# Kernel tuning notes

Measured on AMD Instinct MI355X. Metric: run time of the kernel, lower is better.

The kernel has to match this reference:

```python
import jax, jax.numpy as jnp
import numpy as np

N_NODES = 50000
N_EDGES = 600000
N_FEAT = 128
N_GRAPHS = 256
DIM = 95
N_OUT = 12
N_ITER = 10
BN_EPS = 1e-5


def setup_inputs() -> dict:
    key = jax.random.key(0)
    ks = jax.random.split(key, 16)
    inp = {}
    inp["x"] = jax.random.normal(ks[0], (N_NODES, N_FEAT), dtype=jnp.float32)
    inp["edge_index"] = jax.random.randint(ks[1], (2, N_EDGES), 0, N_NODES, dtype=jnp.int64)
    inp["batch"] = jnp.sort(jax.random.randint(ks[2], (N_NODES,), 0, N_GRAPHS, dtype=jnp.int64))
    def lin(k, fan_in, fan_out):
        bound = 1.0 / np.sqrt(fan_in)
        kw, kb = jax.random.split(k)
        W = jax.random.uniform(kw, (fan_in, fan_out), jnp.float32, -bound, bound)
        b = jax.random.uniform(kb, (fan_out,), jnp.float32, -bound, bound)
        return W, b
    inp["W1a"], inp["b1a"] = lin(ks[3], N_FEAT, N_FEAT)            # nn1 layer 1
    inp["W1b"], inp["b1b"] = lin(ks[4], N_FEAT, N_FEAT)            # nn1 layer 2
    inp["gamma"] = jnp.ones((N_FEAT,), jnp.float32)                 # bn1 weight
    inp["beta"] = jnp.zeros((N_FEAT,), jnp.float32)                 # bn1 bias
    inp["Wl1"], inp["bl1"] = lin(ks[5], 2 * N_FEAT, N_FEAT // 2)   # lin1
    inp["Wl2"], inp["bl2"] = lin(ks[6], 2 * N_FEAT, N_FEAT // 2)   # lin2
    inp["Wm1"], inp["bm1"] = lin(ks[7], N_FEAT, DIM)               # MLP layer 1
    inp["Wm2"], inp["bm2"] = lin(ks[8], DIM, N_OUT)                # MLP layer 2
    return inp


def reference(x, edge_index, batch, W1a, b1a, W1b, b1b, gamma, beta,
              Wl1, bl1, Wl2, bl2, Wm1, bm1, Wm2, bm2):
    src, dst = edge_index[0], edge_index[1]
    # GINConv (eps=0): h_i = nn1(x_i + sum_{j->i} x_j)
    agg = jax.ops.segment_sum(x[src], dst, num_segments=N_NODES)
    h0 = x + agg
    h0 = jax.nn.relu(h0 @ W1a + b1a) @ W1b + b1b
    x1 = jax.nn.relu(h0)
    # BatchNorm1d (training mode: batch statistics, biased variance)
    mean = jnp.mean(x1, axis=0)
    var = jnp.mean(jnp.square(x1 - mean), axis=0)
    x1 = gamma * (x1 - mean) * jax.lax.rsqrt(var + BN_EPS) + beta
    # global_mean_pool over graph ids
    sums = jax.ops.segment_sum(x1, batch, num_segments=N_GRAPHS)
    counts = jax.ops.segment_sum(jnp.ones((N_NODES,), x1.dtype), batch, num_segments=N_GRAPHS)
    xg = sums / jnp.maximum(counts, 1.0)[:, None]
    # recurrent gated loop
    h = xg
    for _ in range(N_ITER):
        cat = jnp.concatenate([xg, h], axis=1)          # [G, 2*F]
        p = cat @ Wl1 + bl1
        q = cat @ Wl2 + bl2
        h = jnp.concatenate([jnp.tanh(q), jax.nn.sigmoid(p)], axis=1)
    # output MLP
    return jax.nn.relu(h @ Wm1 + bm1) @ Wm2 + bm2
```

## Files before the change

kernel.cpp:

```cpp
#include <hip/hip_runtime.h>
#include <cstddef>

#define N_NODES  50000
#define N_EDGES  600000
#define N_FEAT   128
#define N_GRAPHS 256
#define DIMM     95
#define N_OUTD   12
#define N_ITERS  10

#define N_CHUNKS 196

#define WS_STATS 0
#define WS_XG    (WS_STATS + 256)
#define WS_CNT   (WS_XG + N_GRAPHS * N_FEAT)
#define WS_OFF   (WS_CNT + N_NODES)
#define WS_CUR   (WS_OFF + N_NODES + 4)
#define WS_CHS   (WS_CUR + N_NODES)
#define WS_SORT  (WS_CHS + 256)

#define SR 132

__global__ void k_zero(float* __restrict__ ws) {
    int i = blockIdx.x * 256 + threadIdx.x;
    int* cnt = (int*)ws + WS_CNT;
    if (i < N_NODES) cnt[i] = 0;
    if (i < 256) ws[WS_STATS + i] = 0.f;
    if (i < N_GRAPHS * N_FEAT) ws[WS_XG + i] = 0.f;
}

__global__ void k_hist(const int* __restrict__ ei, float* __restrict__ ws) {
    int e = blockIdx.x * 256 + threadIdx.x;
    int* cnt = (int*)ws + WS_CNT;
    if (e < N_EDGES) atomicAdd(&cnt[ei[N_EDGES + e]], 1);
}

__global__ void k_chunk(float* __restrict__ ws) {
    __shared__ int red[4];
    const int tid = threadIdx.x;
    int* cnt = (int*)ws + WS_CNT;
    int i = blockIdx.x * 256 + tid;
    int v = (i < N_NODES) ? cnt[i] : 0;
    #pragma unroll
    for (int d = 32; d; d >>= 1) v += __shfl_down(v, d);
    if ((tid & 63) == 0) red[tid >> 6] = v;
    __syncthreads();
    if (tid == 0) ((int*)ws + WS_CHS)[blockIdx.x] = red[0] + red[1] + red[2] + red[3];
}

__global__ void k_scan0(float* __restrict__ ws) {
    __shared__ int s[256];
    const int tid = threadIdx.x;
    int* chs = (int*)ws + WS_CHS;
    int v = (tid < N_CHUNKS) ? chs[tid] : 0;
    s[tid] = v;
    __syncthreads();
    #pragma unroll
    for (int d = 1; d < 256; d <<= 1) {
        int t = (tid >= d) ? s[tid - d] : 0;
        __syncthreads();
        s[tid] += t;
        __syncthreads();
    }
    if (tid < N_CHUNKS) chs[tid] = s[tid] - v;
    if (tid == 0) ((int*)ws + WS_OFF)[N_NODES] = N_EDGES;
}

__global__ void k_scan1(float* __restrict__ ws) {
    __shared__ int s[256];
    const int tid = threadIdx.x;
    int* cnt = (int*)ws + WS_CNT;
    int* off = (int*)ws + WS_OFF;
    int* cur = (int*)ws + WS_CUR;
    int i = blockIdx.x * 256 + tid;
    int v = (i < N_NODES) ? cnt[i] : 0;
    s[tid] = v;
    __syncthreads();
    #pragma unroll
    for (int d = 1; d < 256; d <<= 1) {
        int t = (tid >= d) ? s[tid - d] : 0;
        __syncthreads();
        s[tid] += t;
        __syncthreads();
    }
    int o = ((int*)ws + WS_CHS)[blockIdx.x] + s[tid] - v;
    if (i < N_NODES) { off[i] = o; cur[i] = o; }
}

__global__ void k_scatter(const int* __restrict__ ei, float* __restrict__ ws) {
    int e = blockIdx.x * 256 + threadIdx.x;
    if (e >= N_EDGES) return;
    int d = ei[N_EDGES + e];
    int s = ei[e];
    int* cur = (int*)ws + WS_CUR;
    int pos = atomicAdd(&cur[d], 1);
    ((int*)ws + WS_SORT)[pos] = s;
}

__global__ __launch_bounds__(256, 4) void k_fused(const float* __restrict__ x,
        const int* __restrict__ batch, float* __restrict__ ws,
        const float* __restrict__ W1a, const float* __restrict__ b1a,
        const float* __restrict__ W1b, const float* __restrict__ b1b) {
    __shared__ float As[64 * SR];
    __shared__ float red[256];
    __shared__ int batch_l[64];
    const int tid  = threadIdx.x;
    const int lane = tid & 63;
    const int wv   = tid >> 6;
    const int fg   = tid & 15;
    const int rg   = tid >> 4;
    const int row0 = blockIdx.x * 64;

    const int* off = (const int*)ws + WS_OFF;
    const int* ss  = (const int*)ws + WS_SORT;

    if (tid < 64) {
        int r = row0 + tid;
        batch_l[tid] = (r < N_NODES) ? batch[r] : (N_GRAPHS - 1);
    }

    for (int ii = 0; ii < 16; ++ii) {
        const int i = wv * 16 + ii;
        const int r = row0 + i;
        float2 acc = make_float2(0.f, 0.f);
        if (r < N_NODES) {
            acc = *(const float2*)(x + (size_t)r * N_FEAT + 2 * lane);
            const int lo = off[r], hi = off[r + 1];
            for (int c0 = lo; c0 < hi; c0 += 64) {
                const int cdeg = min(64, hi - c0);
                int myidx = (lane < cdeg) ? ss[c0 + lane] : 0;
                int j = 0;
                for (; j + 4 <= cdeg; j += 4) {
                    int s0 = __shfl(myidx, j);
                    int s1 = __shfl(myidx, j + 1);
                    int s2 = __shfl(myidx, j + 2);
                    int s3 = __shfl(myidx, j + 3);
                    float2 v0 = *(const float2*)(x + (size_t)s0 * N_FEAT + 2 * lane);
                    float2 v1 = *(const float2*)(x + (size_t)s1 * N_FEAT + 2 * lane);
                    float2 v2 = *(const float2*)(x + (size_t)s2 * N_FEAT + 2 * lane);
                    float2 v3 = *(const float2*)(x + (size_t)s3 * N_FEAT + 2 * lane);
                    acc.x += v0.x + v1.x + v2.x + v3.x;
                    acc.y += v0.y + v1.y + v2.y + v3.y;
                }
                for (; j < cdeg; ++j) {
                    int s = __shfl(myidx, j);
                    float2 v = *(const float2*)(x + (size_t)s * N_FEAT + 2 * lane);
                    acc.x += v.x; acc.y += v.y;
                }
            }
        }
        *(float2*)(As + i * SR + 2 * lane) = acc;
    }
    __syncthreads();

    float acc[4][8];
    #pragma unroll
    for (int i = 0; i < 4; ++i)
        #pragma unroll
        for (int j = 0; j < 8; ++j) acc[i][j] = 0.f;

    #pragma unroll 2
    for (int k = 0; k < N_FEAT; k += 4) {
        float4 w[8];
        #pragma unroll
        for (int kk = 0; kk < 4; ++kk) {
            w[2 * kk]     = *(const float4*)(W1a + (k + kk) * N_FEAT + fg * 8);
            w[2 * kk + 1] = *(const float4*)(W1a + (k + kk) * N_FEAT + fg * 8 + 4);
        }
        #pragma unroll
        for (int i = 0; i < 4; ++i) {
            const float4 a4 = *(const float4*)(As + (rg * 4 + i) * SR + k);
            const float av[4] = {a4.x, a4.y, a4.z, a4.w};
            #pragma unroll
            for (int kk = 0; kk < 4; ++kk) {
                acc[i][0] += av[kk] * w[2 * kk].x;
                acc[i][1] += av[kk] * w[2 * kk].y;
                acc[i][2] += av[kk] * w[2 * kk].z;
                acc[i][3] += av[kk] * w[2 * kk].w;
                acc[i][4] += av[kk] * w[2 * kk + 1].x;
                acc[i][5] += av[kk] * w[2 * kk + 1].y;
                acc[i][6] += av[kk] * w[2 * kk + 1].z;
                acc[i][7] += av[kk] * w[2 * kk + 1].w;
            }
        }
    }
    __syncthreads();

    {
        const float4 ba0 = *(const float4*)(b1a + fg * 8);
        const float4 ba1 = *(const float4*)(b1a + fg * 8 + 4);
        #pragma unroll
        for (int i = 0; i < 4; ++i) {
            float4 u0, u1;
            u0.x = fmaxf(acc[i][0] + ba0.x, 0.f); u0.y = fmaxf(acc[i][1] + ba0.y, 0.f);
            u0.z = fmaxf(acc[i][2] + ba0.z, 0.f); u0.w = fmaxf(acc[i][3] + ba0.w, 0.f);
            u1.x = fmaxf(acc[i][4] + ba1.x, 0.f); u1.y = fmaxf(acc[i][5] + ba1.y, 0.f);
            u1.z = fmaxf(acc[i][6] + ba1.z, 0.f); u1.w = fmaxf(acc[i][7] + ba1.w, 0.f);
            *(float4*)(As + (rg * 4 + i) * SR + fg * 8)     = u0;
            *(float4*)(As + (rg * 4 + i) * SR + fg * 8 + 4) = u1;
        }
    }
    __syncthreads();

    #pragma unroll
    for (int i = 0; i < 4; ++i)
        #pragma unroll
        for (int j = 0; j < 8; ++j) acc[i][j] = 0.f;

    #pragma unroll 2
    for (int k = 0; k < N_FEAT; k += 4) {
        float4 w[8];
        #pragma unroll
        for (int kk = 0; kk < 4; ++kk) {
            w[2 * kk]     = *(const float4*)(W1b + (k + kk) * N_FEAT + fg * 8);
            w[2 * kk + 1] = *(const float4*)(W1b + (k + kk) * N_FEAT + fg * 8 + 4);
        }
        #pragma unroll
        for (int i = 0; i < 4; ++i) {
            const float4 a4 = *(const float4*)(As + (rg * 4 + i) * SR + k);
            const float av[4] = {a4.x, a4.y, a4.z, a4.w};
            #pragma unroll
            for (int kk = 0; kk < 4; ++kk) {
                acc[i][0] += av[kk] * w[2 * kk].x;
                acc[i][1] += av[kk] * w[2 * kk].y;
                acc[i][2] += av[kk] * w[2 * kk].z;
                acc[i][3] += av[kk] * w[2 * kk].w;
                acc[i][4] += av[kk] * w[2 * kk + 1].x;
                acc[i][5] += av[kk] * w[2 * kk + 1].y;
                acc[i][6] += av[kk] * w[2 * kk + 1].z;
                acc[i][7] += av[kk] * w[2 * kk + 1].w;
            }
        }
    }
    __syncthreads();

    {
        const float4 bb0 = *(const float4*)(b1b + fg * 8);
        const float4 bb1 = *(const float4*)(b1b + fg * 8 + 4);
        #pragma unroll
        for (int i = 0; i < 4; ++i) {
            float4 u0, u1;
            u0.x = fmaxf(acc[i][0] + bb0.x, 0.f); u0.y = fmaxf(acc[i][1] + bb0.y, 0.f);
            u0.z = fmaxf(acc[i][2] + bb0.z, 0.f); u0.w = fmaxf(acc[i][3] + bb0.w, 0.f);
            u1.x = fmaxf(acc[i][4] + bb1.x, 0.f); u1.y = fmaxf(acc[i][5] + bb1.y, 0.f);
            u1.z = fmaxf(acc[i][6] + bb1.z, 0.f); u1.w = fmaxf(acc[i][7] + bb1.w, 0.f);
            *(float4*)(As + (rg * 4 + i) * SR + fg * 8)     = u0;
            *(float4*)(As + (rg * 4 + i) * SR + fg * 8 + 4) = u1;
        }
    }
    __syncthreads();

    {
        const int c = tid & 127;
        const int h = tid >> 7;
        float sum = 0.f, sq = 0.f, pool = 0.f;
        int curg = batch_l[h * 32];
        bool any = (row0 + h * 32) < N_NODES;
        #pragma unroll 4
        for (int rr = 0; rr < 32; ++rr) {
            int rl = h * 32 + rr;
            if (row0 + rl >= N_NODES) break;
            float v = As[rl * SR + c];
            int g = batch_l[rl];
            if (g != curg) {
                unsafeAtomicAdd(ws + WS_XG + (size_t)curg * N_FEAT + c, pool);
                pool = 0.f; curg = g;
            }
            sum += v; sq += v * v; pool += v;
        }
        if (any) unsafeAtomicAdd(ws + WS_XG + (size_t)curg * N_FEAT + c, pool);
        if (h == 1) { red[c] = sum; red[128 + c] = sq; }
        __syncthreads();
        if (h == 0) {
            unsafeAtomicAdd(ws + WS_STATS + c, sum + red[c]);
            unsafeAtomicAdd(ws + WS_STATS + 128 + c, sq + red[128 + c]);
        }
    }
}

__device__ __forceinline__ int lbound(const int* __restrict__ a, int n, int v) {
    int lo = 0, hi = n;
    while (lo < hi) { int m = (lo + hi) >> 1; if (a[m] < v) lo = m + 1; else hi = m; }
    return lo;
}

__global__ void k_apply(const int* __restrict__ batch,
                        const float* __restrict__ gamma, const float* __restrict__ beta,
                        float* __restrict__ ws) {
    const int g = blockIdx.x, c = threadIdx.x;
    __shared__ int range[2];
    if (c < 2) range[c] = lbound(batch, N_NODES, g + c);
    __syncthreads();
    const int cnt = range[1] - range[0];
    float mean = ws[WS_STATS + c] * (1.f / N_NODES);
    float var  = fmaxf(ws[WS_STATS + 128 + c] * (1.f / N_NODES) - mean * mean, 0.f);
    float sc = gamma[c] * rsqrtf(var + 1e-5f);
    float sh = beta[c] - mean * sc;
    float pool = ws[WS_XG + (size_t)g * N_FEAT + c];
    ws[WS_XG + (size_t)g * N_FEAT + c] = (cnt > 0) ? (sc * pool / (float)cnt + sh) : 0.f;
}

__global__ __launch_bounds__(256) void k_recur(const float* __restrict__ ws,
        const float* __restrict__ Wl1, const float* __restrict__ bl1,
        const float* __restrict__ Wl2, const float* __restrict__ bl2,
        const float* __restrict__ Wm1, const float* __restrict__ bm1,
        const float* __restrict__ Wm2, const float* __restrict__ bm2,
        float* __restrict__ out) {
    __shared__ float W1h[128 * 64];
    __shared__ float W2h[128 * 64];
    __shared__ float xg_s[128];
    __shared__ float h_s[128];
    __shared__ float px[2][64];
    __shared__ float pq[2][2][64];
    __shared__ float m_s[DIMM];
    const int g = blockIdx.x, tid = threadIdx.x;

    for (int i = tid; i < 128 * 64; i += 256) {
        W1h[i] = Wl1[128 * 64 + i];
        W2h[i] = Wl2[128 * 64 + i];
    }
    if (tid < 128) {
        float v = ws[WS_XG + g * N_FEAT + tid];
        xg_s[tid] = v;
        h_s[tid] = v;
    }
    __syncthreads();

    const int sel  = tid >> 7;
    const int part = (tid >> 6) & 1;
    const int j    = tid & 63;

    {
        const float* Wg = sel ? Wl2 : Wl1;
        float a = 0.f;
        const int k0 = part * 64;
        #pragma unroll 4
        for (int k = 0; k < 64; ++k) a += xg_s[k0 + k] * Wg[(k0 + k) * 64 + j];
        pq[sel][part][j] = a;
    }
    __syncthreads();
    if (part == 0) {
        const float* bias = sel ? bl2 : bl1;
        px[sel][j] = pq[sel][0][j] + pq[sel][1][j] + bias[j];
    }
    __syncthreads();

    const float* Wh = sel ? W2h : W1h;
    for (int it = 0; it < N_ITERS; ++it) {
        float a = 0.f;
        const int k0 = part * 64;
        #pragma unroll
        for (int k = 0; k < 64; k += 4) {
            const float4 h4 = *(const float4*)(h_s + k0 + k);
            a += h4.x * Wh[(k0 + k + 0) * 64 + j];
            a += h4.y * Wh[(k0 + k + 1) * 64 + j];
            a += h4.z * Wh[(k0 + k + 2) * 64 + j];
            a += h4.w * Wh[(k0 + k + 3) * 64 + j];
        }
        pq[sel][part][j] = a;
        __syncthreads();
        if (part == 0) {
            float tot = pq[sel][0][j] + pq[sel][1][j] + px[sel][j];
            if (sel == 0) h_s[64 + j] = 1.f / (1.f + expf(-tot));
            else          h_s[j] = tanhf(tot);
        }
        __syncthreads();
    }

    if (tid < DIMM) {
        float a = bm1[tid];
        #pragma unroll 4
        for (int k = 0; k < 128; ++k) a += h_s[k] * Wm1[k * DIMM + tid];
        m_s[tid] = fmaxf(a, 0.f);
    }
    __syncthreads();
    if (tid < N_OUTD) {
        float a = bm2[tid];
        for (int k = 0; k < DIMM; ++k) a += m_s[k] * Wm2[k * N_OUTD + tid];
        out[g * N_OUTD + tid] = a;
    }
}

extern "C" void kernel_launch(void* const* d_in, const int* in_sizes, int n_in,
                              void* d_out, int out_size, void* d_ws, size_t ws_size,
                              hipStream_t stream) {
    const float* x     = (const float*)d_in[0];
    const int*   ei    = (const int*)d_in[1];
    const int*   batch = (const int*)d_in[2];
    const float* W1a = (const float*)d_in[3];
    const float* b1a = (const float*)d_in[4];
    const float* W1b = (const float*)d_in[5];
    const float* b1b = (const float*)d_in[6];
    const float* gamma = (const float*)d_in[7];
    const float* beta  = (const float*)d_in[8];
    const float* Wl1 = (const float*)d_in[9];
    const float* bl1 = (const float*)d_in[10];
    const float* Wl2 = (const float*)d_in[11];
    const float* bl2 = (const float*)d_in[12];
    const float* Wm1 = (const float*)d_in[13];
    const float* bm1 = (const float*)d_in[14];
    const float* Wm2 = (const float*)d_in[15];
    const float* bm2 = (const float*)d_in[16];
    float* out = (float*)d_out;
    float* ws  = (float*)d_ws;

    k_zero   <<<(N_NODES + 255) / 256, 256, 0, stream>>>(ws);
    k_hist   <<<(N_EDGES + 255) / 256, 256, 0, stream>>>(ei, ws);
    k_chunk  <<<N_CHUNKS, 256, 0, stream>>>(ws);
    k_scan0  <<<1, 256, 0, stream>>>(ws);
    k_scan1  <<<N_CHUNKS, 256, 0, stream>>>(ws);
    k_scatter<<<(N_EDGES + 255) / 256, 256, 0, stream>>>(ei, ws);
    k_fused  <<<(N_NODES + 63) / 64, 256, 0, stream>>>(x, batch, ws, W1a, b1a, W1b, b1b);
    k_apply  <<<N_GRAPHS, 128, 0, stream>>>(batch, gamma, beta, ws);
    k_recur  <<<N_GRAPHS, 256, 0, stream>>>(ws, Wl1, bl1, Wl2, bl2, Wm1, bm1, Wm2, bm2, out);
}
```

Baseline: 311.9 us.

## Interleave four-row neighbor gathers, shrink node tile, fold BN apply into recurrence

```diff
diff --git a/kernel.cpp b/kernel.cpp
--- a/kernel.cpp
+++ b/kernel.cpp
@@ -20,6 +20,7 @@
 #define WS_SORT  (WS_CHS + 256)
 
 #define SR 132
+#define TR 48
 
 __global__ void k_zero(float* __restrict__ ws) {
     int i = blockIdx.x * 256 + threadIdx.x;
@@ -101,61 +102,84 @@
         const int* __restrict__ batch, float* __restrict__ ws,
         const float* __restrict__ W1a, const float* __restrict__ b1a,
         const float* __restrict__ W1b, const float* __restrict__ b1b) {
-    __shared__ float As[64 * SR];
+    __shared__ float As[TR * SR];
     __shared__ float red[256];
-    __shared__ int batch_l[64];
+    __shared__ int batch_l[TR];
     const int tid  = threadIdx.x;
     const int lane = tid & 63;
     const int wv   = tid >> 6;
     const int fg   = tid & 15;
     const int rg   = tid >> 4;
-    const int row0 = blockIdx.x * 64;
+    const int row0 = blockIdx.x * TR;
 
     const int* off = (const int*)ws + WS_OFF;
     const int* ss  = (const int*)ws + WS_SORT;
-
-    if (tid < 64) {
+    const float2* __restrict__ x2 = (const float2*)x;
+
+    if (tid < TR) {
         int r = row0 + tid;
         batch_l[tid] = (r < N_NODES) ? batch[r] : (N_GRAPHS - 1);
     }
 
-    for (int ii = 0; ii < 16; ++ii) {
-        const int i = wv * 16 + ii;
-        const int r = row0 + i;
-        float2 acc = make_float2(0.f, 0.f);
-        if (r < N_NODES) {
-            acc = *(const float2*)(x + (size_t)r * N_FEAT + 2 * lane);
-            const int lo = off[r], hi = off[r + 1];
-            for (int c0 = lo; c0 < hi; c0 += 64) {
-                const int cdeg = min(64, hi - c0);
-                int myidx = (lane < cdeg) ? ss[c0 + lane] : 0;
-                int j = 0;
-                for (; j + 4 <= cdeg; j += 4) {
-                    int s0 = __shfl(myidx, j);
-                    int s1 = __shfl(myidx, j + 1);
-                    int s2 = __shfl(myidx, j + 2);
-                    int s3 = __shfl(myidx, j + 3);
-                    float2 v0 = *(const float2*)(x + (size_t)s0 * N_FEAT + 2 * lane);
-                    float2 v1 = *(const float2*)(x + (size_t)s1 * N_FEAT + 2 * lane);
-                    float2 v2 = *(const float2*)(x + (size_t)s2 * N_FEAT + 2 * lane);
-                    float2 v3 = *(const float2*)(x + (size_t)s3 * N_FEAT + 2 * lane);
-                    acc.x += v0.x + v1.x + v2.x + v3.x;
-                    acc.y += v0.y + v1.y + v2.y + v3.y;
+    for (int ii = 0; ii < 12; ii += 4) {
+        int lo[4], deg[4], idxv[4];
+        float2 acc[4];
+        #pragma unroll
+        for (int t = 0; t < 4; ++t) {
+            const int r = row0 + wv * 12 + ii + t;
+            const bool valid = r < N_NODES;
+            lo[t] = valid ? off[r] : 0;
+            int hi = valid ? off[r + 1] : 0;
+            deg[t] = hi - lo[t];
+            acc[t] = valid ? x2[(size_t)r * 64 + lane] : make_float2(0.f, 0.f);
+            idxv[t] = (lane < min(deg[t], 64)) ? ss[lo[t] + lane] : 0;
+        }
+        const int dmax = min(max(max(deg[0], deg[1]), max(deg[2], deg[3])), 64);
+        for (int j = 0; j < dmax; j += 2) {
+            float2 v[8];
+            #pragma unroll
+            for (int t = 0; t < 4; ++t) {
+                if (j < deg[t]) {
+                    int s = __shfl(idxv[t], j);
+                    v[t] = x2[(size_t)s * 64 + lane];
+                } else v[t] = make_float2(0.f, 0.f);
+            }
+            #pragma unroll
+            for (int t = 0; t < 4; ++t) {
+                if (j + 1 < deg[t]) {
+                    int s = __shfl(idxv[t], j + 1);
+                    v[4 + t] = x2[(size_t)s * 64 + lane];
+                } else v[4 + t] = make_float2(0.f, 0.f);
+            }
+            #pragma unroll
+            for (int t = 0; t < 4; ++t) {
+                acc[t].x += v[t].x + v[4 + t].x;
+                acc[t].y += v[t].y + v[4 + t].y;
+            }
+        }
+        #pragma unroll
+        for (int t = 0; t < 4; ++t) {
+            if (deg[t] > 64) {
+                for (int c0 = lo[t] + 64; c0 < lo[t] + deg[t]; c0 += 64) {
+                    const int cd = min(64, lo[t] + deg[t] - c0);
+                    int mi = (lane < cd) ? ss[c0 + lane] : 0;
+                    for (int j = 0; j < cd; ++j) {
+                        int s = __shfl(mi, j);
+                        float2 vv = x2[(size_t)s * 64 + lane];
+                        acc[t].x += vv.x; acc[t].y += vv.y;
+                    }
                 }
-                for (; j < cdeg; ++j) {
-                    int s = __shfl(myidx, j);
-                    float2 v = *(const float2*)(x + (size_t)s * N_FEAT + 2 * lane);
-                    acc.x += v.x; acc.y += v.y;
-                }
-            }
-        }
-        *(float2*)(As + i * SR + 2 * lane) = acc;
-    }
-    __syncthreads();
-
-    float acc[4][8];
+            }
+        }
+        #pragma unroll
+        for (int t = 0; t < 4; ++t)
+            *(float2*)(As + (wv * 12 + ii + t) * SR + 2 * lane) = acc[t];
+    }
+    __syncthreads();
+
+    float acc[3][8];
     #pragma unroll
-    for (int i = 0; i < 4; ++i)
+    for (int i = 0; i < 3; ++i)
         #pragma unroll
         for (int j = 0; j < 8; ++j) acc[i][j] = 0.f;
 
@@ -168,8 +192,8 @@
             w[2 * kk + 1] = *(const float4*)(W1a + (k + kk) * N_FEAT + fg * 8 + 4);
         }
         #pragma unroll
-        for (int i = 0; i < 4; ++i) {
-            const float4 a4 = *(const float4*)(As + (rg * 4 + i) * SR + k);
+        for (int i = 0; i < 3; ++i) {
+            const float4 a4 = *(const float4*)(As + (rg * 3 + i) * SR + k);
             const float av[4] = {a4.x, a4.y, a4.z, a4.w};
             #pragma unroll
             for (int kk = 0; kk < 4; ++kk) {
@@ -190,20 +214,20 @@
         const float4 ba0 = *(const float4*)(b1a + fg * 8);
         const float4 ba1 = *(const float4*)(b1a + fg * 8 + 4);
         #pragma unroll
-        for (int i = 0; i < 4; ++i) {
+        for (int i = 0; i < 3; ++i) {
             float4 u0, u1;
             u0.x = fmaxf(acc[i][0] + ba0.x, 0.f); u0.y = fmaxf(acc[i][1] + ba0.y, 0.f);
             u0.z = fmaxf(acc[i][2] + ba0.z, 0.f); u0.w = fmaxf(acc[i][3] + ba0.w, 0.f);
             u1.x = fmaxf(acc[i][4] + ba1.x, 0.f); u1.y = fmaxf(acc[i][5] + ba1.y, 0.f);
             u1.z = fmaxf(acc[i][6] + ba1.z, 0.f); u1.w = fmaxf(acc[i][7] + ba1.w, 0.f);
-            *(float4*)(As + (rg * 4 + i) * SR + fg * 8)     = u0;
-            *(float4*)(As + (rg * 4 + i) * SR + fg * 8 + 4) = u1;
+            *(float4*)(As + (rg * 3 + i) * SR + fg * 8)     = u0;
+            *(float4*)(As + (rg * 3 + i) * SR + fg * 8 + 4) = u1;
         }
     }
     __syncthreads();
 
     #pragma unroll
-    for (int i = 0; i < 4; ++i)
+    for (int i = 0; i < 3; ++i)
         #pragma unroll
         for (int j = 0; j < 8; ++j) acc[i][j] = 0.f;
 
@@ -216,8 +240,8 @@
             w[2 * kk + 1] = *(const float4*)(W1b + (k + kk) * N_FEAT + fg * 8 + 4);
         }
         #pragma unroll
-        for (int i = 0; i < 4; ++i) {
-            const float4 a4 = *(const float4*)(As + (rg * 4 + i) * SR + k);
+        for (int i = 0; i < 3; ++i) {
+            const float4 a4 = *(const float4*)(As + (rg * 3 + i) * SR + k);
             const float av[4] = {a4.x, a4.y, a4.z, a4.w};
             #pragma unroll
             for (int kk = 0; kk < 4; ++kk) {
@@ -238,14 +262,14 @@
         const float4 bb0 = *(const float4*)(b1b + fg * 8);
         const float4 bb1 = *(const float4*)(b1b + fg * 8 + 4);
         #pragma unroll
-        for (int i = 0; i < 4; ++i) {
+        for (int i = 0; i < 3; ++i) {
             float4 u0, u1;
             u0.x = fmaxf(acc[i][0] + bb0.x, 0.f); u0.y = fmaxf(acc[i][1] + bb0.y, 0.f);
             u0.z = fmaxf(acc[i][2] + bb0.z, 0.f); u0.w = fmaxf(acc[i][3] + bb0.w, 0.f);
             u1.x = fmaxf(acc[i][4] + bb1.x, 0.f); u1.y = fmaxf(acc[i][5] + bb1.y, 0.f);
             u1.z = fmaxf(acc[i][6] + bb1.z, 0.f); u1.w = fmaxf(acc[i][7] + bb1.w, 0.f);
-            *(float4*)(As + (rg * 4 + i) * SR + fg * 8)     = u0;
-            *(float4*)(As + (rg * 4 + i) * SR + fg * 8 + 4) = u1;
+            *(float4*)(As + (rg * 3 + i) * SR + fg * 8)     = u0;
+            *(float4*)(As + (rg * 3 + i) * SR + fg * 8 + 4) = u1;
         }
     }
     __syncthreads();
@@ -254,11 +278,11 @@
         const int c = tid & 127;
         const int h = tid >> 7;
         float sum = 0.f, sq = 0.f, pool = 0.f;
-        int curg = batch_l[h * 32];
-        bool any = (row0 + h * 32) < N_NODES;
+        int curg = batch_l[h * 24];
+        bool any = (row0 + h * 24) < N_NODES;
         #pragma unroll 4
-        for (int rr = 0; rr < 32; ++rr) {
-            int rl = h * 32 + rr;
+        for (int rr = 0; rr < 24; ++rr) {
+            int rl = h * 24 + rr;
             if (row0 + rl >= N_NODES) break;
             float v = As[rl * SR + c];
             int g = batch_l[rl];
@@ -284,23 +308,9 @@
     return lo;
 }
 
-__global__ void k_apply(const int* __restrict__ batch,
-                        const float* __restrict__ gamma, const float* __restrict__ beta,
-                        float* __restrict__ ws) {
-    const int g = blockIdx.x, c = threadIdx.x;
-    __shared__ int range[2];
-    if (c < 2) range[c] = lbound(batch, N_NODES, g + c);
-    __syncthreads();
-    const int cnt = range[1] - range[0];
-    float mean = ws[WS_STATS + c] * (1.f / N_NODES);
-    float var  = fmaxf(ws[WS_STATS + 128 + c] * (1.f / N_NODES) - mean * mean, 0.f);
-    float sc = gamma[c] * rsqrtf(var + 1e-5f);
-    float sh = beta[c] - mean * sc;
-    float pool = ws[WS_XG + (size_t)g * N_FEAT + c];
-    ws[WS_XG + (size_t)g * N_FEAT + c] = (cnt > 0) ? (sc * pool / (float)cnt + sh) : 0.f;
-}
-
 __global__ __launch_bounds__(256) void k_recur(const float* __restrict__ ws,
+        const int* __restrict__ batch,
+        const float* __restrict__ gamma, const float* __restrict__ beta,
         const float* __restrict__ Wl1, const float* __restrict__ bl1,
         const float* __restrict__ Wl2, const float* __restrict__ bl2,
         const float* __restrict__ Wm1, const float* __restrict__ bm1,
@@ -313,14 +323,23 @@
     __shared__ float px[2][64];
     __shared__ float pq[2][2][64];
     __shared__ float m_s[DIMM];
+    __shared__ int range[2];
     const int g = blockIdx.x, tid = threadIdx.x;
 
+    if (tid < 2) range[tid] = lbound(batch, N_NODES, g + tid);
     for (int i = tid; i < 128 * 64; i += 256) {
         W1h[i] = Wl1[128 * 64 + i];
         W2h[i] = Wl2[128 * 64 + i];
     }
+    __syncthreads();
     if (tid < 128) {
-        float v = ws[WS_XG + g * N_FEAT + tid];
+        const int cnt = range[1] - range[0];
+        float mean = ws[WS_STATS + tid] * (1.f / N_NODES);
+        float var  = fmaxf(ws[WS_STATS + 128 + tid] * (1.f / N_NODES) - mean * mean, 0.f);
+        float sc = gamma[tid] * rsqrtf(var + 1e-5f);
+        float sh = beta[tid] - mean * sc;
+        float pool = ws[WS_XG + (size_t)g * N_FEAT + tid];
+        float v = (cnt > 0) ? (sc * pool / (float)cnt + sh) : 0.f;
         xg_s[tid] = v;
         h_s[tid] = v;
     }
@@ -410,7 +429,7 @@
     k_scan0  <<<1, 256, 0, stream>>>(ws);
     k_scan1  <<<N_CHUNKS, 256, 0, stream>>>(ws);
     k_scatter<<<(N_EDGES + 255) / 256, 256, 0, stream>>>(ei, ws);
-    k_fused  <<<(N_NODES + 63) / 64, 256, 0, stream>>>(x, batch, ws, W1a, b1a, W1b, b1b);
-    k_apply  <<<N_GRAPHS, 128, 0, stream>>>(batch, gamma, beta, ws);
-    k_recur  <<<N_GRAPHS, 256, 0, stream>>>(ws, Wl1, bl1, Wl2, bl2, Wm1, bm1, Wm2, bm2, out);
-}
+    k_fused  <<<(N_NODES + TR - 1) / TR, 256, 0, stream>>>(x, batch, ws, W1a, b1a, W1b, b1b);
+    k_recur  <<<N_GRAPHS, 256, 0, stream>>>(ws, batch, gamma, beta,
+                                            Wl1, bl1, Wl2, bl2, Wm1, bm1, Wm2, bm2, out);
+}
```

Measured after the change: 313.5 us. About the same (+0.5%).
